# Performance work log

Measured on AMD Instinct MI355X. Metric: run time of the kernel, lower is better.

Reference implementation:

```python
import jax, jax.numpy as jnp
import numpy as np

B, T, N, C = 4, 6, 512, 8
HID, FEAT, EMB, IN_DIM = 64, 16, 32, 1
KS, KC, HORIZON = 3, 2, 3
ALPHA = 3.0

def _init(key, shape):
    fin = shape[-2] if len(shape) >= 2 else shape[-1]
    return jax.random.normal(key, shape, dtype=jnp.float32) * (1.0 / fin) ** 0.5

def setup_inputs():
    ks = jax.random.split(jax.random.key(0), 32)
    L_enc = (IN_DIM + FEAT + HID) * KS * KC
    L_dec = (HID + FEAT + HID) * KS * KC
    return {
        "X_seq": jax.random.normal(ks[0], (B, T, N, C), dtype=jnp.float32),
        "As": jax.random.uniform(ks[1], (N, N), dtype=jnp.float32) / N,
        "Ac": jax.random.uniform(ks[2], (C, C), dtype=jnp.float32) / C,
        "feature": jax.random.normal(ks[3], (N, FEAT), dtype=jnp.float32),
        "Wu_S": _init(ks[4], (C, HID)), "Wv_S": _init(ks[5], (C, HID)),
        "Wu_C": _init(ks[6], (N, HID)), "Wv_C": _init(ks[7], (N, HID)),
        "mfS_w1": _init(ks[8], (4, 2, 256)), "mfS_b1": jnp.zeros((4, 256), jnp.float32),
        "mfS_w2": _init(ks[9], (4, 256, 256)), "mfS_b2": jnp.zeros((4, 256), jnp.float32),
        "mfC_w1": _init(ks[10], (4, 2, 256)), "mfC_b1": jnp.zeros((4, 256), jnp.float32),
        "mfC_w2": _init(ks[11], (4, 256, 256)), "mfC_b2": jnp.zeros((4, 256), jnp.float32),
        "enc_gW": _init(ks[12], (L_enc, 2 * HID)), "enc_gb": jnp.zeros((2 * HID,), jnp.float32),
        "enc_cW": _init(ks[13], (L_enc, HID)), "enc_cb": jnp.zeros((HID,), jnp.float32),
        "dec_gW": _init(ks[14], (L_dec, 2 * HID)), "dec_gb": jnp.zeros((2 * HID,), jnp.float32),
        "dec_cW": _init(ks[15], (L_dec, HID)), "dec_cb": jnp.zeros((HID,), jnp.float32),
        "out_w1": _init(ks[16], (HID, EMB)), "out_b1": jnp.zeros((EMB,), jnp.float32),
        "out_w2": _init(ks[17], (EMB, IN_DIM)), "out_b2": jnp.zeros((IN_DIM,), jnp.float32),
    }

def _mlp(x, w1, b1, w2, b2):
    return jax.nn.relu(x @ w1 + b1) @ w2 + b2

def _mixed_fusion(A, P, w1, b1, w2, b2):
    # node_feat = [rowsum(A), rowsum(P)]; key/value MLPs indexed 0:key_A 1:key_P 2:val_A 3:val_P
    nf = jnp.stack([A.sum(-1), P.sum(-1)], axis=-1)            # [n, 2]
    An, Pn = A @ nf, P @ nf
    key = _mlp(An, w1[0], b1[0], w2[0], b2[0]) + _mlp(Pn, w1[1], b1[1], w2[1], b2[1])
    val = _mlp(An, w1[2], b1[2], w2[2], b2[2]) + _mlp(Pn, w1[3], b1[3], w2[3], b2[3])
    a = jax.nn.sigmoid(key @ val.T)
    return a * A + (1.0 - a) * P

def _adaptive_graph(Xf, Wu, Wv):
    U = jnp.tanh(ALPHA * Xf @ Wu)                              # [b,t,n,h]
    V = jnp.tanh(ALPHA * Xf @ Wv)
    M = jnp.einsum('btnh,btmh->nm', U, V)
    # Ps = softmax(relu(M - M^T)) matches einsum pair in torch source
    return jax.nn.softmax(jax.nn.relu(M - M.T), axis=-1)

def _cheby(G, K):
    mats = [jnp.eye(G.shape[0], dtype=G.dtype), G]
    for _ in range(2, K):
        mats.append(2.0 * G @ mats[-1] - mats[-2])
    return jnp.stack(mats[:K], axis=0)                         # [K, n, n]

def _bdg(X, Gs_set, Gc_set, W, b):
    # X: [b,n,c,l]; fused Ks x Kc Chebyshev mode products; cat order (k, j, l) matches torch cat
    t1 = jnp.einsum('bncl,knm->kbmcl', X, Gs_set)
    t2 = jnp.einsum('kbmcl,jcd->bmdkjl', t1, Gc_set)
    feat = t2.reshape(t2.shape[0], t2.shape[1], t2.shape[2], -1)
    return feat @ W + b

def _cell(Xt, Ht, featx, Gs_set, Gc_set, gW, gb, cW, cb):
    XH = jnp.concatenate([Xt, Ht, featx], axis=-1)
    uv = _bdg(XH, Gs_set, Gc_set, gW, gb)
    update = jax.nn.sigmoid(uv[..., :HID])
    reset = jax.nn.sigmoid(uv[..., HID:])
    cand_in = jnp.concatenate([Xt, reset * Ht, featx], axis=-1)
    cand = jnp.tanh(_bdg(cand_in, Gs_set, Gc_set, cW, cb))
    return (1.0 - update) * Ht + update * cand

def _forward(X_seq, As, Ac, feature, Wu_S, Wv_S, Wu_C, Wv_C,
             mfS_w1, mfS_b1, mfS_w2, mfS_b2, mfC_w1, mfC_b1, mfC_w2, mfC_b2,
             enc_gW, enc_gb, enc_cW, enc_cb, dec_gW, dec_gb, dec_cW, dec_cb,
             out_w1, out_b1, out_w2, out_b2):
    # MGP_Gen: adaptive spatial / categorical graphs fused with priors
    Ps = _adaptive_graph(X_seq, Wu_S, Wv_S)
    Gs = _mixed_fusion(As, Ps, mfS_w1, mfS_b1, mfS_w2, mfS_b2)
    Xc = jnp.swapaxes(X_seq, 2, 3)                             # [b,t,c,n]
    Pc = _adaptive_graph(Xc, Wu_C, Wv_C)
    Gc = _mixed_fusion(Ac, Pc, mfC_w1, mfC_b1, mfC_w2, mfC_b2)
    Gs_set, Gc_set = _cheby(Gs, KS), _cheby(Gc, KC)
    featx = jnp.broadcast_to(feature[None, :, None, :], (B, N, C, FEAT))
    X5 = X_seq[..., None]                                      # [b,t,n,c,1]
    Ht = jnp.zeros((B, N, C, HID), dtype=X_seq.dtype)
    for t in range(T):                                         # encoder GRU over history
        Ht = _cell(X5[:, t], Ht, featx, Gs_set, Gc_set, enc_gW, enc_gb, enc_cW, enc_cb)
    deco_in, Hd = Ht, Ht
    outs = []
    for _ in range(HORIZON):
        Hd = _cell(deco_in, Hd, featx, Gs_set, Gc_set, dec_gW, dec_gb, dec_cW, dec_cb)
        outs.append(_mlp(Hd, out_w1, out_b1, out_w2, out_b2))
        deco_in = Hd
    return jnp.stack(outs, axis=1)                             # [b, horizon, n, c, 1]

def reference(X_seq, As, Ac, feature, Wu_S, Wv_S, Wu_C, Wv_C, mfS_w1, mfS_b1, mfS_w2, mfS_b2, mfC_w1, mfC_b1, mfC_w2, mfC_b2, enc_gW, enc_gb, enc_cW, enc_cb, dec_gW, dec_gb, dec_cW, dec_cb, out_w1, out_b1, out_w2, out_b2):
    return _forward(X_seq, As, Ac, feature, Wu_S, Wv_S, Wu_C, Wv_C, mfS_w1, mfS_b1, mfS_w2, mfS_b2, mfC_w1, mfC_b1, mfC_w2, mfC_b2, enc_gW, enc_gb, enc_cW, enc_cb, dec_gW, dec_gb, dec_cW, dec_cb, out_w1, out_b1, out_w2, out_b2)
```

## Files before the change

### kernel.cpp

```cpp
#include <hip/hip_runtime.h>
#include <math.h>

constexpr int kB = 4, kT = 6, kN = 512, kC = 8;
constexpr int kH = 64, kF = 16, kE = 32;
constexpr int kKS = 3, kKC = 2, kHOR = 3;
constexpr int kBT = kB * kT;
constexpr int kRK = kBT * kH;
constexpr int L_ENC = 1 + kH + kF;
constexpr int L_DEC = kH + kH + kF;
constexpr int PL_ENC = 96;
constexpr int PL_DEC = 160;
constexpr int KP_ENC = 3 * PL_ENC;
constexpr int KP_DGF = 288;
constexpr int KP_DEC = 3 * PL_DEC;
constexpr float kALPHA = 3.0f;

typedef unsigned short ushortT;
typedef short short8 __attribute__((ext_vector_type(8)));
typedef float f32x4 __attribute__((ext_vector_type(4)));

__device__ __forceinline__ float sigm(float x) { return 1.0f / (1.0f + __expf(-x)); }

__device__ __forceinline__ ushortT f2bf(float f) {
    union { float f; unsigned int u; } v; v.f = f;
    unsigned int r = v.u + 0x7fffu + ((v.u >> 16) & 1u);
    return (ushortT)(r >> 16);
}

__device__ __forceinline__ void fma44(const float4& a, const float4& b, float acc[4][4]) {
    acc[0][0] += a.x*b.x; acc[0][1] += a.x*b.y; acc[0][2] += a.x*b.z; acc[0][3] += a.x*b.w;
    acc[1][0] += a.y*b.x; acc[1][1] += a.y*b.y; acc[1][2] += a.y*b.z; acc[1][3] += a.y*b.w;
    acc[2][0] += a.z*b.x; acc[2][1] += a.z*b.y; acc[2][2] += a.z*b.z; acc[2][3] += a.z*b.w;
    acc[3][0] += a.w*b.x; acc[3][1] += a.w*b.y; acc[3][2] += a.w*b.z; acc[3][3] += a.w*b.w;
}

__global__ __launch_bounds__(256) void k_prep_all(
    const float* __restrict__ egW, const float* __restrict__ ecW,
    const float* __restrict__ dgW, const float* __restrict__ dcW,
    const float* __restrict__ w2, const float* __restrict__ w2C,
    ushortT* __restrict__ WTg_e, ushortT* __restrict__ WTc_e,
    ushortT* __restrict__ WTg_d, ushortT* __restrict__ WTc_d,
    float* __restrict__ w2tK, float* __restrict__ w2tV, float* __restrict__ w2tC)
{
    int idx = blockIdx.x * 256 + threadIdx.x;
    if (idx < 73728) {
        int qp = idx % KP_ENC, o = idx / KP_ENC;
        int kk = qp / PL_ENC, l = qp - kk * PL_ENC;
        int lo = (l < 64) ? l + 1 : (l == 64) ? 0 : (l < 80) ? L_ENC : (l - 15);
        int j = o / 128, oo = o - j * 128;
        float v = (lo < L_ENC) ? egW[(size_t)((kk*2 + j)*L_ENC + lo) * 128 + oo] : 0.f;
        WTg_e[idx] = f2bf(v);
    } else if (idx < 110592) {
        int r = idx - 73728;
        int qp = r % KP_ENC, o = r / KP_ENC;
        int kk = qp / PL_ENC, l = qp - kk * PL_ENC;
        int lo = (l < 64) ? l + 1 : (l == 64) ? 0 : (l < 80) ? L_ENC : (l - 15);
        int j = o / 64, oo = o - j * 64;
        float v = (lo < L_ENC) ? ecW[(size_t)((kk*2 + j)*L_ENC + lo) * 64 + oo] : 0.f;
        WTc_e[r] = f2bf(v);
    } else if (idx < 184320) {
        int r = idx - 110592;
        int qp = r % KP_DGF, o = r / KP_DGF;
        int k = qp / 96, p = qp - k * 96;
        int j = o >> 7, oo = o & 127;
        int base = (k*2 + j) * L_DEC;
        float v;
        if (p < 64)      v = dgW[(size_t)(base + p)*128 + oo] + dgW[(size_t)(base + 64 + p)*128 + oo];
        else if (p < 80) v = dgW[(size_t)(base + 128 + (p - 64))*128 + oo];
        else             v = 0.f;
        WTg_d[r] = f2bf(v);
    } else if (idx < 245760) {
        int r = idx - 184320;
        int qp = r % KP_DEC, o = r / KP_DEC;
        int kk = qp / PL_DEC, l = qp - kk * PL_DEC;
        int j = o / 64, oo = o - j * 64;
        float v = (l < L_DEC) ? dcW[(size_t)((kk*2 + j)*L_DEC + l) * 64 + oo] : 0.f;
        WTc_d[r] = f2bf(v);
    } else if (idx < 376832) {
        int r = idx - 245760;
        int kk = r & 511, n = r >> 9;
        int j = kk >> 8, k = kk & 255;
        w2tK[r] = w2[(size_t)(0 + j)*65536 + k*256 + n];
        w2tV[r] = w2[(size_t)(2 + j)*65536 + k*256 + n];
    } else if (idx < 638976) {
        int r = idx - 376832;
        int q = r >> 16; int rem = r & 65535;
        int oc = rem >> 8, k = rem & 255;
        w2tC[r] = w2C[(size_t)q*65536 + k*256 + oc];
    }
}


__global__ __launch_bounds__(256) void k_uvproj_s_nfa(
    const float* __restrict__ X, const float* __restrict__ Wu, const float* __restrict__ Wv,
    const float* __restrict__ As,
    float* __restrict__ Upr, float* __restrict__ Vpr, float* __restrict__ nf)
{
    if (blockIdx.x >= 3072) {
        int i = blockIdx.x - 3072, tid = threadIdx.x;
        __shared__ float sa[256];
        float a = 0.f;
        for (int j = tid; j < kN; j += 256) a += As[(size_t)i*kN + j];
        sa[tid] = a; __syncthreads();
        for (int s = 128; s > 0; s >>= 1) { if (tid < s) sa[tid] += sa[tid+s]; __syncthreads(); }
        if (!tid) { nf[i*2] = sa[0]; nf[i*2+1] = 1.0f; }
        return;
    }
    int idx = blockIdx.x * 256 + threadIdx.x;
    int h = idx % kH; int bt = (idx / kH) % kBT; int n = idx / (kH * kBT);
    const float* xr = X + ((size_t)bt * kN + n) * kC;
    float u = 0.f, v = 0.f;
#pragma unroll
    for (int c = 0; c < kC; ++c) { float x = xr[c]; u += x * Wu[c*kH + h]; v += x * Wv[c*kH + h]; }
    Upr[(size_t)n * kRK + bt * kH + h] = tanhf(kALPHA * u);
    Vpr[(size_t)n * kRK + bt * kH + h] = tanhf(kALPHA * v);
}

__global__ __launch_bounds__(512) void k_uvproj_c2(
    const float* __restrict__ X, const float* __restrict__ WuC, const float* __restrict__ WvC,
    float* __restrict__ Uc, float* __restrict__ Vc)
{
    __shared__ float Xs[4096];
    __shared__ float Wus[4096], Wvs[4096];
    int bt = blockIdx.x, tid = threadIdx.x;
    for (int i = tid; i < 4096; i += 512) Xs[i] = X[(size_t)bt*4096 + i];
    int c = tid >> 6, h = tid & 63;
    float u = 0.f, v = 0.f;
    for (int n0 = 0; n0 < 512; n0 += 64) {
        __syncthreads();
        for (int i = tid; i < 4096; i += 512) { Wus[i] = WuC[n0*64 + i]; Wvs[i] = WvC[n0*64 + i]; }
        __syncthreads();
#pragma unroll 8
        for (int nn = 0; nn < 64; ++nn) {
            float x = Xs[(n0+nn)*8 + c];
            u += x * Wus[nn*64 + h];
            v += x * Wvs[nn*64 + h];
        }
    }
    Uc[(size_t)bt*512 + c*64 + h] = tanhf(kALPHA * u);
    Vc[(size_t)bt*512 + c*64 + h] = tanhf(kALPHA * v);
}

__global__ __launch_bounds__(256) void k_softmax_anpn(
    const float* __restrict__ part, const float* __restrict__ A, const float* __restrict__ nf,
    float* __restrict__ P, float* __restrict__ An, float* __restrict__ Pn)
{
    int i = blockIdx.x, tid = threadIdx.x;
    __shared__ float s0[256], s1[256], s2[256], s3[256], s4[256];
    auto mval = [&](int r, int c2) -> float {
        size_t id = (size_t)r*kN + c2;
        return part[id] + part[262144 + id] + part[524288 + id] + part[786432 + id];
    };
    float mx = -1e30f;
    for (int j = tid; j < kN; j += 256)
        mx = fmaxf(mx, fmaxf(mval(i, j) - mval(j, i), 0.f));
    s0[tid] = mx; __syncthreads();
    for (int s = 128; s > 0; s >>= 1) { if (tid < s) s0[tid] = fmaxf(s0[tid], s0[tid+s]); __syncthreads(); }
    mx = s0[0]; __syncthreads();
    float sum=0, pn0=0, pn1=0, an0=0, an1=0;
    for (int j = tid; j < kN; j += 256) {
        float v = fmaxf(mval(i, j) - mval(j, i), 0.f);
        float e = __expf(v - mx);
        P[(size_t)i*kN + j] = e;
        float n0 = nf[2*j], n1 = nf[2*j+1];
        float a = A[(size_t)i*kN + j];
        sum += e; pn0 += e*n0; pn1 += e*n1; an0 += a*n0; an1 += a*n1;
    }
    s0[tid]=sum; s1[tid]=pn0; s2[tid]=pn1; s3[tid]=an0; s4[tid]=an1; __syncthreads();
    for (int s = 128; s > 0; s >>= 1) {
        if (tid < s) { s0[tid]+=s0[tid+s]; s1[tid]+=s1[tid+s]; s2[tid]+=s2[tid+s]; s3[tid]+=s3[tid+s]; s4[tid]+=s4[tid+s]; }
        __syncthreads();
    }
    float inv = 1.f / s0[0];
    if (!tid) { Pn[i*2] = s1[0]*inv; Pn[i*2+1] = s2[0]*inv; An[i*2] = s3[0]; An[i*2+1] = s4[0]; }
    __syncthreads();
    for (int j = tid; j < kN; j += 256) P[(size_t)i*kN + j] *= inv;
}

__global__ __launch_bounds__(256) void k_mlp1kv(
    const float* __restrict__ An, const float* __restrict__ Pn,
    const float* __restrict__ w1, const float* __restrict__ b1, float* __restrict__ hid)
{
    int idx = blockIdx.x * 256 + threadIdx.x;
    if (idx >= 524288) return;
    int half = idx >> 18;
    int r = idx & 262143;
    int col = r & 511, i = r >> 9;
    int ia = half*2, ip = half*2 + 1;
    float v;
    if (col < 256) {
        const float* w = w1 + (size_t)ia * 512;
        v = An[i*2]*w[col] + An[i*2+1]*w[256 + col] + b1[ia*256 + col];
    } else {
        int o = col - 256;
        const float* w = w1 + (size_t)ip * 512;
        v = Pn[i*2]*w[o] + Pn[i*2+1]*w[256 + o] + b1[ip*256 + o];
    }
    hid[idx] = fmaxf(v, 0.f);
}

__global__ __launch_bounds__(256) void k_gemm_ntsk(
    const float* __restrict__ A, const float* __restrict__ B, float* __restrict__ part,
    int M, int N, int K, int skl)
{
    __shared__ __align__(16) float sA[32][68];
    __shared__ __align__(16) float sB[32][68];
    int tid = threadIdx.x, tx = tid & 15, ty = tid >> 4;
    int j0 = blockIdx.x * 64, i0 = blockIdx.y * 64;
    int kb = blockIdx.z * skl;
    float acc[4][4] = {};
    for (int k0 = kb; k0 < kb + skl; k0 += 32) {
#pragma unroll
        for (int it = 0; it < 2; ++it) {
            int q = tid + it * 256;
            int row = q >> 3, ks = (q & 7) * 4;
            float4 va = *(const float4*)&A[(size_t)(i0 + row)*K + k0 + ks];
            float4 vb = *(const float4*)&B[(size_t)(j0 + row)*K + k0 + ks];
            sA[ks+0][row] = va.x; sA[ks+1][row] = va.y; sA[ks+2][row] = va.z; sA[ks+3][row] = va.w;
            sB[ks+0][row] = vb.x; sB[ks+1][row] = vb.y; sB[ks+2][row] = vb.z; sB[ks+3][row] = vb.w;
        }
        __syncthreads();
#pragma unroll
        for (int kk = 0; kk < 32; ++kk) {
            float4 a = *(const float4*)&sA[kk][ty*4];
            float4 b = *(const float4*)&sB[kk][tx*4];
            fma44(a, b, acc);
        }
        __syncthreads();
    }
    float* dst = part + (size_t)blockIdx.z * M * N;
#pragma unroll
    for (int i = 0; i < 4; ++i)
#pragma unroll
        for (int j = 0; j < 4; ++j)
            dst[(size_t)(i0 + ty*4 + i)*N + j0 + tx*4 + j] = acc[i][j];
}

__global__ __launch_bounds__(256) void k_ntsk_kv2(
    const float* __restrict__ hid, const float* __restrict__ w2t,
    const float* __restrict__ b2, float* __restrict__ keyval)
{
    __shared__ __align__(16) float sA[32][68];
    __shared__ __align__(16) float sB[32][68];
    int tid = threadIdx.x, tx = tid & 15, ty = tid >> 4;
    int z = blockIdx.z;
    const float* A = hid + (size_t)z * 262144;
    const float* B = w2t + (size_t)z * 131072;
    int j0 = blockIdx.x * 64, i0 = blockIdx.y * 64;
    float acc[4][4] = {};
    for (int k0 = 0; k0 < 512; k0 += 32) {
#pragma unroll
        for (int it = 0; it < 2; ++it) {
            int q = tid + it * 256;
            int row = q >> 3, ks = (q & 7) * 4;
            float4 va = *(const float4*)&A[(size_t)(i0 + row)*512 + k0 + ks];
            float4 vb = *(const float4*)&B[(size_t)(j0 + row)*512 + k0 + ks];
            sA[ks+0][row] = va.x; sA[ks+1][row] = va.y; sA[ks+2][row] = va.z; sA[ks+3][row] = va.w;
            sB[ks+0][row] = vb.x; sB[ks+1][row] = vb.y; sB[ks+2][row] = vb.z; sB[ks+3][row] = vb.w;
        }
        __syncthreads();
#pragma unroll
        for (int kk = 0; kk < 32; ++kk) {
            float4 a = *(const float4*)&sA[kk][ty*4];
            float4 b = *(const float4*)&sB[kk][tx*4];
            fma44(a, b, acc);
        }
        __syncthreads();
    }
    float* dst = keyval + (size_t)z * 131072;
#pragma unroll
    for (int i = 0; i < 4; ++i)
#pragma unroll
        for (int j = 0; j < 4; ++j) {
            int col = j0 + tx*4 + j;
            dst[(size_t)(i0 + ty*4 + i)*256 + col] = acc[i][j] + b2[z*512 + col] + b2[z*512 + 256 + col];
        }
}

__global__ void k_fuse_transp(
    const float* __restrict__ part, const float* __restrict__ As,
    const float* __restrict__ Ps, ushortT* __restrict__ Gt)
{
    __shared__ float tile[32][33];
    int bx = blockIdx.x * 32, by = blockIdx.y * 32;
    int x = threadIdx.x, y0 = threadIdx.y;
    for (int yy = y0; yy < 32; yy += 8) {
        size_t id = (size_t)(by + yy)*kN + bx + x;
        float s = part[id] + part[262144 + id];
        float a = sigm(s);
        tile[yy][x] = a*As[id] + (1.f - a)*Ps[id];
    }
    __syncthreads();
    for (int yy = y0; yy < 32; yy += 8) Gt[(size_t)(bx+yy)*kN + by + x] = f2bf(tile[x][yy]);
}

__global__ __launch_bounds__(256) void k_cheby64(
    const ushortT* __restrict__ Gst, ushortT* __restrict__ Gst2)
{
    __shared__ short sA[64][40];
    __shared__ short sB[64][40];
    int tid = threadIdx.x;
    int m0 = blockIdx.y * 64, j0 = blockIdx.x * 64;
    int w = tid >> 6, lane = tid & 63;
    f32x4 acc[4];
#pragma unroll
    for (int i = 0; i < 4; ++i) acc[i] = (f32x4){0.f, 0.f, 0.f, 0.f};
    for (int k0 = 0; k0 < kN; k0 += 32) {
        {
            int row = tid >> 2, lc = (tid & 3) * 8;
            *(short8*)&sA[row][lc] = *(const short8*)(Gst + (size_t)(m0 + row)*kN + k0 + lc);
        }
        {
            int kr = tid & 31, jc = (tid >> 5) * 8;
            short8 v = *(const short8*)(Gst + (size_t)(k0 + kr)*kN + j0 + jc);
#pragma unroll
            for (int i = 0; i < 8; ++i) sB[jc + i][kr] = v[i];
        }
        __syncthreads();
        short8 bf = *(const short8*)&sB[w*16 + (lane & 15)][(lane >> 4) * 8];
#pragma unroll
        for (int mi = 0; mi < 4; ++mi) {
            short8 af = *(const short8*)&sA[mi*16 + (lane & 15)][(lane >> 4) * 8];
            acc[mi] = __builtin_amdgcn_mfma_f32_16x16x32_bf16(af, bf, acc[mi], 0, 0, 0);
        }
        __syncthreads();
    }
#pragma unroll
    for (int mi = 0; mi < 4; ++mi) {
        int row0 = m0 + mi*16 + (lane >> 4)*4;
        int col = j0 + w*16 + (lane & 15);
#pragma unroll
        for (int q = 0; q < 4; ++q) {
            int row = row0 + q;
            Gst2[(size_t)row*kN + col] = f2bf(2.f*acc[mi][q] - (row == col ? 1.f : 0.f));
        }
    }
}

__device__ __forceinline__ void cat_front2(
    const float* __restrict__ Uc, const float* __restrict__ Vc, const float* __restrict__ Ac,
    float* UVs , float* red ,
    float* McS, float* Pcs, float* rsA, float* Ans, float* Pns)
{
    int tid = threadIdx.x;
    int cd = tid >> 2, kc = tid & 3;
    int c = cd >> 3, d = cd & 7;
    float s = 0.f;
    for (int bt0 = 0; bt0 < kBT; bt0 += 4) {
        __syncthreads();
        for (int i = tid; i < 2048; i += 256) {
            UVs[i]        = Uc[(size_t)bt0*512 + i];
            UVs[2048 + i] = Vc[(size_t)bt0*512 + i];
        }
        __syncthreads();
#pragma unroll
        for (int bt = 0; bt < 4; ++bt)
#pragma unroll
            for (int hh = 0; hh < 16; ++hh) {
                int h = kc*16 + hh;
                s += UVs[bt*512 + c*64 + h] * UVs[2048 + bt*512 + d*64 + h];
            }
    }
    red[tid] = s; __syncthreads();
    if (tid < 64) McS[tid] = red[tid*4] + red[tid*4+1] + red[tid*4+2] + red[tid*4+3];
    __syncthreads();
    if (tid < 8) {
        int i = tid;
        float row[8]; float mx = -1e30f;
#pragma unroll
        for (int j = 0; j < 8; ++j) { float v = fmaxf(McS[i*8+j] - McS[j*8+i], 0.f); row[j] = v; mx = fmaxf(mx, v); }
        float s2 = 0.f;
#pragma unroll
        for (int j = 0; j < 8; ++j) { row[j] = __expf(row[j] - mx); s2 += row[j]; }
        float inv = 1.f / s2;
#pragma unroll
        for (int j = 0; j < 8; ++j) Pcs[i*8+j] = row[j] * inv;
        float a = 0.f;
#pragma unroll
        for (int j = 0; j < 8; ++j) a += Ac[i*8+j];
        rsA[i] = a;
    }
    __syncthreads();
    if (tid < 16) {
        int i = tid >> 1, comp = tid & 1;
        float an = 0.f, pn = 0.f;
#pragma unroll
        for (int j = 0; j < 8; ++j) {
            float nfj = comp ? 1.f : rsA[j];
            an += Ac[i*8+j] * nfj; pn += Pcs[i*8+j] * nfj;
        }
        Ans[i*2+comp] = an; Pns[i*2+comp] = pn;
    }
    __syncthreads();
}

__global__ __launch_bounds__(256) void k_catmlp4(
    const float* __restrict__ Uc, const float* __restrict__ Vc, const float* __restrict__ Ac,
    const float* __restrict__ w1, const float* __restrict__ b1,
    const float* __restrict__ w2tC, const float* __restrict__ b2,
    float* __restrict__ keyval)
{
    __shared__ float UVs[4096];
    __shared__ float red[256];
    __shared__ float McS[64], Pcs[64], rsA[8], Ans[16], Pns[16];
    __shared__ float hA[8][260], hP[8][260];
    int tid = threadIdx.x;
    int kv = blockIdx.x, c0 = blockIdx.y * 32;
    int qa = kv*2, qp = kv*2 + 1;
    cat_front2(Uc, Vc, Ac, UVs, red, McS, Pcs, rsA, Ans, Pns);
    for (int e = tid; e < 2048; e += 256) {
        int i = e >> 8, o = e & 255;
        hA[i][o] = fmaxf(Ans[i*2]*w1[qa*512 + o] + Ans[i*2+1]*w1[qa*512 + 256 + o] + b1[qa*256 + o], 0.f);
        hP[i][o] = fmaxf(Pns[i*2]*w1[qp*512 + o] + Pns[i*2+1]*w1[qp*512 + 256 + o] + b1[qp*256 + o], 0.f);
    }
    __syncthreads();
    int i = tid >> 5, ocl = tid & 31, oc = c0 + ocl;
    float s = b2[qa*256 + oc] + b2[qp*256 + oc];
    const float* wa = w2tC + (size_t)qa*65536 + (size_t)oc*256;
    const float* wp = w2tC + (size_t)qp*65536 + (size_t)oc*256;
#pragma unroll 4
    for (int k = 0; k < 256; k += 4) {
        float4 va = *(const float4*)&wa[k];
        float4 vp = *(const float4*)&wp[k];
        float4 ha = *(const float4*)&hA[i][k];
        float4 hp = *(const float4*)&hP[i][k];
        s += va.x*ha.x + va.y*ha.y + va.z*ha.z + va.w*ha.w
           + vp.x*hp.x + vp.y*hp.y + vp.z*hp.z + vp.w*hp.w;
    }
    keyval[(size_t)kv*2048 + i*256 + oc] = s;
}

__global__ __launch_bounds__(256) void k_gcfuse4(
    const float* __restrict__ keyval,
    const float* __restrict__ Uc, const float* __restrict__ Vc, const float* __restrict__ Ac,
    float* __restrict__ GcF)
{
    __shared__ float UVs[4096];
    __shared__ float red[256];
    __shared__ float McS[64], Pcs[64], rsA[8], Ans[16], Pns[16];
    __shared__ float dotp[256];
    int tid = threadIdx.x;
    cat_front2(Uc, Vc, Ac, UVs, red, McS, Pcs, rsA, Ans, Pns);
    int cd = tid >> 2, kc = tid & 3;
    int c = cd >> 3, d = cd & 7;
    const float* key = keyval;
    const float* val = keyval + 2048;
    float s = 0.f;
#pragma unroll 4
    for (int k = kc*64; k < kc*64 + 64; k += 4) {
        float4 k4 = *(const float4*)&key[c*256 + k];
        float4 v4 = *(const float4*)&val[d*256 + k];
        s += k4.x*v4.x + k4.y*v4.y + k4.z*v4.z + k4.w*v4.w;
    }
    dotp[tid] = s; __syncthreads();
    if (tid < 64) {
        float t = dotp[tid*4] + dotp[tid*4+1] + dotp[tid*4+2] + dotp[tid*4+3];
        float a = sigm(t);
        GcF[tid] = a*Ac[tid] + (1.f - a)*Pcs[tid];
    }
}

template<int CLP, int PL, int ACTW, int OFF>
__global__ __launch_bounds__(256) void k_t1m(
    const ushortT* __restrict__ Gst, const ushortT* __restrict__ Xin, ushortT* __restrict__ Yout)
{
    __shared__ short sA[128][40];
    __shared__ short sB[128][40];
    int tid = threadIdx.x;
    int ki = blockIdx.z >> 2, b = blockIdx.z & 3;
    const ushortT* A = Gst + (size_t)ki * kN * kN;
    const ushortT* B = Xin + (size_t)b * kN * CLP;
    ushortT* C = Yout + (size_t)(ki*4 + b) * kN * CLP;
    int m0 = blockIdx.y * 128, j0 = blockIdx.x * 128;
    int w = tid >> 6, lane = tid & 63, wr = w >> 1, wc = w & 1;
    int kr = tid & 31, jc = (tid >> 5) * 8;
    int colr0, colr1;
    { int j = j0 + jc;      int cg = j / ACTW; colr0 = cg*PL + OFF + (j - cg*ACTW); }
    { int j = j0 + jc + 64; int cg = j / ACTW; colr1 = cg*PL + OFF + (j - cg*ACTW); }
    f32x4 acc[4][4];
#pragma unroll
    for (int i = 0; i < 4; ++i)
#pragma unroll
        for (int j = 0; j < 4; ++j) acc[i][j] = (f32x4){0.f, 0.f, 0.f, 0.f};

    for (int k0 = 0; k0 < kN; k0 += 32) {
        {
            int row = tid >> 1, lc = (tid & 1) * 16;
            const ushortT* p = A + (size_t)(m0 + row)*kN + k0 + lc;
            *(short8*)&sA[row][lc]     = *(const short8*)p;
            *(short8*)&sA[row][lc + 8] = *(const short8*)(p + 8);
        }
        {
            short8 v0 = *(const short8*)(B + (size_t)(k0 + kr)*CLP + colr0);
            short8 v1 = *(const short8*)(B + (size_t)(k0 + kr)*CLP + colr1);
#pragma unroll
            for (int i = 0; i < 8; ++i) sB[jc + i][kr] = v0[i];
#pragma unroll
            for (int i = 0; i < 8; ++i) sB[jc + 64 + i][kr] = v1[i];
        }
        __syncthreads();
        short8 af[4], bfr[4];
#pragma unroll
        for (int mi = 0; mi < 4; ++mi)
            af[mi] = *(const short8*)&sA[wr*64 + mi*16 + (lane & 15)][(lane >> 4) * 8];
#pragma unroll
        for (int ni = 0; ni < 4; ++ni)
            bfr[ni] = *(const short8*)&sB[wc*64 + ni*16 + (lane & 15)][(lane >> 4) * 8];
#pragma unroll
        for (int mi = 0; mi < 4; ++mi)
#pragma unroll
            for (int ni = 0; ni < 4; ++ni)
                acc[mi][ni] = __builtin_amdgcn_mfma_f32_16x16x32_bf16(af[mi], bfr[ni], acc[mi][ni], 0, 0, 0);
        __syncthreads();
    }
#pragma unroll
    for (int mi = 0; mi < 4; ++mi) {
#pragma unroll
        for (int ni = 0; ni < 4; ++ni) {
            int row = m0 + wr*64 + mi*16 + (lane >> 4) * 4;
            int fj = j0 + wc*64 + ni*16;
            int cg = fj / ACTW;
            int col = cg*PL + OFF + (fj - cg*ACTW) + (lane & 15);
#pragma unroll
            for (int q = 0; q < 4; ++q)
                C[(size_t)(row + q)*CLP + col] = f2bf(acc[mi][ni][q]);
        }
    }
}

template<int PL, int NQ, int MODE, int FN>
__global__ __launch_bounds__(256) void k_gg(
    const ushortT* __restrict__ XH, const ushortT* __restrict__ Yb,
    const ushortT* __restrict__ WT, float* __restrict__ Cout)
{
    constexpr int BN = 32 * FN;
    constexpr int KP = NQ * 32;
    constexpr int Ntot = 64 * FN;
    __shared__ short sA[128][40];
    __shared__ short sB[BN][40];
    int tid = threadIdx.x;
    int r0 = blockIdx.y * 128, j0 = blockIdx.x * BN;
    int b = r0 >> 12, rr = r0 & 4095;
    const ushortT* src0 = XH + (size_t)r0 * PL;
    const ushortT* src1 = Yb + ((size_t)b       * 4096 + rr) * PL;
    const ushortT* src2 = Yb + ((size_t)(4 + b) * 4096 + rr) * PL;
    int w = tid >> 6, lane = tid & 63, wr = w >> 1, wc = w & 1;
    f32x4 acc[4][FN];
#pragma unroll
    for (int i = 0; i < 4; ++i)
#pragma unroll
        for (int j = 0; j < FN; ++j) acc[i][j] = (f32x4){0.f, 0.f, 0.f, 0.f};

    for (int q = 0; q < NQ; ++q) {
        int k, off;
        if (MODE == 0)      { k = q/3; off = (q - k*3)*32; }
        else if (MODE == 1) { k = q/3; int part = q - k*3; off = (part < 2) ? part*32 : 128; }
        else                { k = q/5; off = (q - k*5)*32; }
        const ushortT* Ap = (k == 0) ? src0 : (k == 1) ? src1 : src2;
        {
            int row = tid >> 1, lc = (tid & 1) * 16;
            const ushortT* p = Ap + (size_t)row * PL + off + lc;
            *(short8*)&sA[row][lc]     = *(const short8*)p;
            *(short8*)&sA[row][lc + 8] = *(const short8*)(p + 8);
        }
        if (FN == 4) {
            int col = tid >> 1, seg = (tid & 1) * 16;
            const ushortT* p = WT + (size_t)(j0 + col)*KP + q*32 + seg;
            *(short8*)&sB[col][seg]     = *(const short8*)p;
            *(short8*)&sB[col][seg + 8] = *(const short8*)(p + 8);
        } else {
            int col = tid >> 2, seg = (tid & 3) * 8;
            *(short8*)&sB[col][seg] = *(const short8*)(WT + (size_t)(j0 + col)*KP + q*32 + seg);
        }
        __syncthreads();
        short8 af[4], bfr[FN];
#pragma unroll
        for (int mi = 0; mi < 4; ++mi)
            af[mi] = *(const short8*)&sA[wr*64 + mi*16 + (lane & 15)][(lane >> 4) * 8];
#pragma unroll
        for (int ni = 0; ni < FN; ++ni)
            bfr[ni] = *(const short8*)&sB[wc*16*FN + ni*16 + (lane & 15)][(lane >> 4) * 8];
#pragma unroll
        for (int mi = 0; mi < 4; ++mi)
#pragma unroll
            for (int ni = 0; ni < FN; ++ni)
                acc[mi][ni] = __builtin_amdgcn_mfma_f32_16x16x32_bf16(af[mi], bfr[ni], acc[mi][ni], 0, 0, 0);
        __syncthreads();
    }
#pragma unroll
    for (int mi = 0; mi < 4; ++mi) {
#pragma unroll
        for (int ni = 0; ni < FN; ++ni) {
            int row = r0 + wr*64 + mi*16 + (lane >> 4) * 4;
            int col = j0 + wc*16*FN + ni*16 + (lane & 15);
#pragma unroll
            for (int q = 0; q < 4; ++q)
                Cout[(size_t)(row + q)*Ntot + col] = acc[mi][ni][q];
        }
    }
}


template<int PL, int XOFF>
__global__ __launch_bounds__(256) void k_gates_ep(
    const float* __restrict__ Gg, const float* __restrict__ GcM,
    const float* __restrict__ gb, const float* __restrict__ Ht,
    float* __restrict__ upd, ushortT* __restrict__ XH)
{
    __shared__ float sG[8][256];
    __shared__ float GcS[64];
    int tid = threadIdx.x, bm = blockIdx.x;
    const float* src = Gg + (size_t)bm * 2048;
    for (int i = tid; i < 2048; i += 256) sG[i >> 8][i & 255] = src[i];
    if (tid < 64) GcS[tid] = GcM[tid];
    __syncthreads();
    int d = tid >> 5, o0 = (tid & 31) * 4;
    size_t rb = (size_t)bm * 8 + d;
#pragma unroll
    for (int q = 0; q < 4; ++q) {
        int o = o0 + q;
        float pre = sG[d][o] + gb[o];
#pragma unroll
        for (int c = 0; c < 8; ++c) pre += GcS[c*8 + d] * sG[c][128 + o];
        float g = sigm(pre);
        if (o < kH) upd[rb*kH + o] = g;
        else {
            int h = o - kH;
            XH[rb*PL + XOFF + h] = f2bf(g * Ht[rb*kH + h]);
        }
    }
}

template<int MODE>
__global__ __launch_bounds__(256) void k_cand_ep(
    const float* __restrict__ Gc2, const float* __restrict__ GcM,
    const float* __restrict__ cb, const float* __restrict__ upd,
    float* __restrict__ Ht, ushortT* __restrict__ XHo,
    const float* __restrict__ X, int tnext,
    const float* __restrict__ ow1, const float* __restrict__ ob1,
    const float* __restrict__ ow2, const float* __restrict__ ob2,
    float* __restrict__ out, int hz)
{
    __shared__ float sG[8][128];
    __shared__ float GcS[64];
    __shared__ float Hn[8][65];
    __shared__ float Pp[8][32];
    int tid = threadIdx.x, bm = blockIdx.x;
    const float* src = Gc2 + (size_t)bm * 1024;
    for (int i = tid; i < 1024; i += 256) sG[i >> 7][i & 127] = src[i];
    if (tid < 64) GcS[tid] = GcM[tid];
    __syncthreads();
    int d = tid >> 5, o0 = (tid & 31) * 2;
    size_t rb = (size_t)bm * 8 + d;
#pragma unroll
    for (int jj = 0; jj < 2; ++jj) {
        int o = o0 + jj;
        float pre = sG[d][o] + cb[o];
#pragma unroll
        for (int c = 0; c < 8; ++c) pre += GcS[c*8 + d] * sG[c][64 + o];
        float cv = tanhf(pre);
        float u = upd[rb*kH + o];
        float h0 = Ht[rb*kH + o];
        float hn = (1.f - u)*h0 + u*cv;
        Ht[rb*kH + o] = hn;
        if (MODE >= 2) Hn[d][o] = hn;
        if (MODE == 0)      XHo[rb*PL_ENC + o] = f2bf(hn);
        else if (MODE <= 2) XHo[rb*PL_DEC + o] = f2bf(hn);
    }
    if (MODE == 0) {
        if (tid < 8) {
            int r = bm*8 + tid;
            int c2 = r & 7, m = (r >> 3) & 511, b2 = r >> 12;
            XHo[(size_t)r*PL_ENC + 64] = f2bf(X[(((size_t)b2*kT + tnext)*kN + m)*kC + c2]);
        }
    }
    if (MODE >= 2) {
        __syncthreads();
        int row = tid >> 5, e = tid & 31;
        float s = ob1[e];
#pragma unroll
        for (int k = 0; k < kH; ++k) s += Hn[row][k] * ow1[k*kE + e];
        Pp[row][e] = fmaxf(s, 0.f) * ow2[e];
        __syncthreads();
        if (tid < 8) {
            float v = ob2[0];
#pragma unroll
            for (int e2 = 0; e2 < 32; ++e2) v += Pp[tid][e2];
            int r = bm*8 + tid;
            int c2 = r & 7, m = (r >> 3) & 511, b2 = r >> 12;
            out[((size_t)(b2*kHOR + hz)*kN + m)*kC + c2] = v;
        }
    }
}

__global__ __launch_bounds__(256) void k_build_init(
    const float* __restrict__ X, const float* __restrict__ featr,
    ushortT* __restrict__ XHe, ushortT* __restrict__ XHd, float* __restrict__ Ht)
{
    int idx = blockIdx.x * 256 + threadIdx.x;
    if (idx < 1572864) {
        int l = idx % PL_ENC; int r = idx / PL_ENC;
        float v;
        if (l < 64)       v = 0.f;
        else if (l == 64) { int c = r & 7, m = (r >> 3) & 511, b = r >> 12; v = X[(((size_t)b*kT)*kN + m)*kC + c]; }
        else if (l < 80)  v = 0.f;
        else              { int m = (r >> 3) & 511; v = featr[m*kF + (l - 80)]; }
        XHe[idx] = f2bf(v);
    } else if (idx < 2097152) {
        int r2 = idx - 1572864;
        int l2 = r2 & 31; int r = r2 >> 5;
        float v = (l2 < 16) ? featr[((r >> 3) & 511)*kF + l2] : 0.f;
        XHd[(size_t)r*PL_DEC + 128 + l2] = f2bf(v);
    } else if (idx < 3145728) {
        Ht[idx - 2097152] = 0.f;
    }
}

extern "C" void kernel_launch(void* const* d_in, const int* in_sizes, int n_in,
                              void* d_out, int out_size, void* d_ws, size_t ws_size,
                              hipStream_t stream)
{
    (void)in_sizes; (void)n_in; (void)out_size; (void)ws_size;
    const float* X      = (const float*)d_in[0];
    const float* As     = (const float*)d_in[1];
    const float* Ac     = (const float*)d_in[2];
    const float* featr  = (const float*)d_in[3];
    const float* WuS    = (const float*)d_in[4];
    const float* WvS    = (const float*)d_in[5];
    const float* WuC    = (const float*)d_in[6];
    const float* WvC    = (const float*)d_in[7];
    const float* mfS_w1 = (const float*)d_in[8];
    const float* mfS_b1 = (const float*)d_in[9];
    const float* mfS_w2 = (const float*)d_in[10];
    const float* mfS_b2 = (const float*)d_in[11];
    const float* mfC_w1 = (const float*)d_in[12];
    const float* mfC_b1 = (const float*)d_in[13];
    const float* mfC_w2 = (const float*)d_in[14];
    const float* mfC_b2 = (const float*)d_in[15];
    const float* enc_gW = (const float*)d_in[16];
    const float* enc_gb = (const float*)d_in[17];
    const float* enc_cW = (const float*)d_in[18];
    const float* enc_cb = (const float*)d_in[19];
    const float* dec_gW = (const float*)d_in[20];
    const float* dec_gb = (const float*)d_in[21];
    const float* dec_cW = (const float*)d_in[22];
    const float* dec_cb = (const float*)d_in[23];
    const float* out_w1 = (const float*)d_in[24];
    const float* out_b1 = (const float*)d_in[25];
    const float* out_w2 = (const float*)d_in[26];
    const float* out_b2 = (const float*)d_in[27];
    float* out = (float*)d_out;
    float* ws = (float*)d_ws;

    float* Ht     = ws;
    float* updb   = Ht + 1048576;
    float* Gg     = updb + 1048576;
    float* Gs_pad = Gg + 4194304;
    float* smallf = Gs_pad + 262144;
    float* nfS = smallf;
    float* AnS = nfS + 1024;
    float* PnS = AnS + 1024;
    float* GcF = PnS + 1024;
    float* kvC = GcF + 64;
    ushortT* XHb  = (ushortT*)(smallf + 8192);
    ushortT* Yb   = XHb + 2621440;
    ushortT* GstB = Yb + 5242880;
    ushortT* WTg_e = GstB + 524288;
    ushortT* WTc_e = WTg_e + 73728;
    ushortT* WTg_d = WTc_e + 36864;
    ushortT* WTc_d = WTg_d + 122880;
    ushortT* XHd   = WTc_d + 61440;
    float* Upr   = Gg;
    float* Vpr   = Upr + 786432;
    float* part  = Vpr + 786432;
    float* Ps    = part + 1048576;
    float* hidKV = Ps + 262144;
    float* keyval= hidKV + 524288;
    float* w2tKV = keyval + 262144;
    float* w2tC  = w2tKV + 262144;
    float* Uc    = updb;
    float* Vc    = Uc + 12288;

    constexpr int CLP_ENC = kC * PL_ENC;
    constexpr int CLP_DEC = kC * PL_DEC;

    k_prep_all<<<2496, 256, 0, stream>>>(enc_gW, enc_cW, dec_gW, dec_cW, mfS_w2, mfC_w2,
                                         WTg_e, WTc_e, WTg_d, WTc_d,
                                         w2tKV, w2tKV + 131072, w2tC);

    k_uvproj_s_nfa<<<3584, 256, 0, stream>>>(X, WuS, WvS, As, Upr, Vpr, nfS);
    k_gemm_ntsk<<<dim3(8, 8, 4), 256, 0, stream>>>(Upr, Vpr, part, 512, 512, 1536, 384);
    k_softmax_anpn<<<kN, 256, 0, stream>>>(part, As, nfS, Ps, AnS, PnS);
    k_mlp1kv<<<2048, 256, 0, stream>>>(AnS, PnS, mfS_w1, mfS_b1, hidKV);
    k_ntsk_kv2<<<dim3(4, 8, 2), 256, 0, stream>>>(hidKV, w2tKV, mfS_b2, keyval);
    k_gemm_ntsk<<<dim3(8, 8, 2), 256, 0, stream>>>(keyval, keyval + 131072, part, 512, 512, 256, 128);
    k_fuse_transp<<<dim3(16, 16), dim3(32, 8), 0, stream>>>(part, As, Ps, GstB);
    k_cheby64<<<dim3(8, 8), 256, 0, stream>>>(GstB, GstB + 262144);

    k_uvproj_c2<<<kBT, 512, 0, stream>>>(X, WuC, WvC, Uc, Vc);
    k_catmlp4<<<dim3(2, 8), 256, 0, stream>>>(Uc, Vc, Ac, mfC_w1, mfC_b1, w2tC, mfC_b2, kvC);
    k_gcfuse4<<<1, 256, 0, stream>>>(kvC, Uc, Vc, Ac, GcF);

    k_build_init<<<12288, 256, 0, stream>>>(X, featr, XHb, XHd, Ht);

    for (int t = 0; t < kT; ++t) {
        if (t == 0)
            k_t1m<CLP_ENC, PL_ENC, 96, 0><<<dim3(6, 4, 8), 256, 0, stream>>>(GstB, XHb, Yb);
        else
            k_t1m<CLP_ENC, PL_ENC, 80, 0><<<dim3(5, 4, 8), 256, 0, stream>>>(GstB, XHb, Yb);
        k_gg<PL_ENC, 9, 0, 4><<<dim3(2, 128), 256, 0, stream>>>(XHb, Yb, WTg_e, Gg);
        k_gates_ep<PL_ENC, 0><<<2048, 256, 0, stream>>>(Gg, GcF, enc_gb, Ht, updb, XHb);
        k_t1m<CLP_ENC, PL_ENC, 64, 0><<<dim3(4, 4, 8), 256, 0, stream>>>(GstB, XHb, Yb);
        k_gg<PL_ENC, 9, 0, 2><<<dim3(2, 128), 256, 0, stream>>>(XHb, Yb, WTc_e, Gg);
        if (t < kT - 1)
            k_cand_ep<0><<<2048, 256, 0, stream>>>(Gg, GcF, enc_cb, updb, Ht, XHb, X, t + 1,
                                                   nullptr, nullptr, nullptr, nullptr, nullptr, 0);
        else
            k_cand_ep<1><<<2048, 256, 0, stream>>>(Gg, GcF, enc_cb, updb, Ht, XHd, nullptr, 0,
                                                   nullptr, nullptr, nullptr, nullptr, nullptr, 0);
    }

    k_t1m<CLP_DEC, PL_DEC, 16, 128><<<dim3(1, 4, 8), 256, 0, stream>>>(GstB, XHd, Yb);
    for (int hz = 0; hz < kHOR; ++hz) {
        k_t1m<CLP_DEC, PL_DEC, 64, 0><<<dim3(4, 4, 8), 256, 0, stream>>>(GstB, XHd, Yb);
        k_gg<PL_DEC, 9, 1, 4><<<dim3(2, 128), 256, 0, stream>>>(XHd, Yb, WTg_d, Gg);
        k_gates_ep<PL_DEC, 64><<<2048, 256, 0, stream>>>(Gg, GcF, dec_gb, Ht, updb, XHd);
        k_t1m<CLP_DEC, PL_DEC, 64, 64><<<dim3(4, 4, 8), 256, 0, stream>>>(GstB, XHd, Yb);
        k_gg<PL_DEC, 15, 2, 2><<<dim3(2, 128), 256, 0, stream>>>(XHd, Yb, WTc_d, Gg);
        if (hz < kHOR - 1)
            k_cand_ep<2><<<2048, 256, 0, stream>>>(Gg, GcF, dec_cb, updb, Ht, XHd, nullptr, 0,
                                                   out_w1, out_b1, out_w2, out_b2, out, hz);
        else
            k_cand_ep<3><<<2048, 256, 0, stream>>>(Gg, GcF, dec_cb, updb, Ht, XHd, nullptr, 0,
                                                   out_w1, out_b1, out_w2, out_b2, out, hz);
    }
}
```

Measured before the change: 926.0 us.

## Merge front-end prep kernels and fuse spatial/channel graph stages into fewer launches

Folds weight prep, spatial and channel UV projections, row sums and state init into a single k_front launch. The Upr·Vpr partial GEMM is merged with the channel cat-MLP in k_p2, and the softmax is merged with the channel gate fusion in k_p3. In the decoder, the static feature-column product is folded into the first gate-side graph multiply through extra blocks. The aim is fewer kernel launches and serial dependency points, with independent work running concurrently inside one grid. The cost is heterogeneous blocks in each launch and shared-memory unions that may limit occupancy.

New measurement: 916.2 us. No clear change (-1.0%).

```diff
diff --git a/kernel.cpp b/kernel.cpp
--- a/kernel.cpp
+++ b/kernel.cpp
@@ -34,148 +34,323 @@
     acc[3][0] += a.w*b.x; acc[3][1] += a.w*b.y; acc[3][2] += a.w*b.z; acc[3][3] += a.w*b.w;
 }
 
-__global__ __launch_bounds__(256) void k_prep_all(
+__global__ __launch_bounds__(256) void k_front(
     const float* __restrict__ egW, const float* __restrict__ ecW,
     const float* __restrict__ dgW, const float* __restrict__ dcW,
     const float* __restrict__ w2, const float* __restrict__ w2C,
+    const float* __restrict__ X, const float* __restrict__ Wu, const float* __restrict__ Wv,
+    const float* __restrict__ As, const float* __restrict__ WuC, const float* __restrict__ WvC,
+    const float* __restrict__ featr,
     ushortT* __restrict__ WTg_e, ushortT* __restrict__ WTc_e,
     ushortT* __restrict__ WTg_d, ushortT* __restrict__ WTc_d,
-    float* __restrict__ w2tK, float* __restrict__ w2tV, float* __restrict__ w2tC)
-{
-    int idx = blockIdx.x * 256 + threadIdx.x;
-    if (idx < 73728) {
-        int qp = idx % KP_ENC, o = idx / KP_ENC;
-        int kk = qp / PL_ENC, l = qp - kk * PL_ENC;
-        int lo = (l < 64) ? l + 1 : (l == 64) ? 0 : (l < 80) ? L_ENC : (l - 15);
-        int j = o / 128, oo = o - j * 128;
-        float v = (lo < L_ENC) ? egW[(size_t)((kk*2 + j)*L_ENC + lo) * 128 + oo] : 0.f;
-        WTg_e[idx] = f2bf(v);
-    } else if (idx < 110592) {
-        int r = idx - 73728;
-        int qp = r % KP_ENC, o = r / KP_ENC;
-        int kk = qp / PL_ENC, l = qp - kk * PL_ENC;
-        int lo = (l < 64) ? l + 1 : (l == 64) ? 0 : (l < 80) ? L_ENC : (l - 15);
-        int j = o / 64, oo = o - j * 64;
-        float v = (lo < L_ENC) ? ecW[(size_t)((kk*2 + j)*L_ENC + lo) * 64 + oo] : 0.f;
-        WTc_e[r] = f2bf(v);
-    } else if (idx < 184320) {
-        int r = idx - 110592;
-        int qp = r % KP_DGF, o = r / KP_DGF;
-        int k = qp / 96, p = qp - k * 96;
-        int j = o >> 7, oo = o & 127;
-        int base = (k*2 + j) * L_DEC;
-        float v;
-        if (p < 64)      v = dgW[(size_t)(base + p)*128 + oo] + dgW[(size_t)(base + 64 + p)*128 + oo];
-        else if (p < 80) v = dgW[(size_t)(base + 128 + (p - 64))*128 + oo];
-        else             v = 0.f;
-        WTg_d[r] = f2bf(v);
-    } else if (idx < 245760) {
-        int r = idx - 184320;
-        int qp = r % KP_DEC, o = r / KP_DEC;
-        int kk = qp / PL_DEC, l = qp - kk * PL_DEC;
-        int j = o / 64, oo = o - j * 64;
-        float v = (l < L_DEC) ? dcW[(size_t)((kk*2 + j)*L_DEC + l) * 64 + oo] : 0.f;
-        WTc_d[r] = f2bf(v);
-    } else if (idx < 376832) {
-        int r = idx - 245760;
-        int kk = r & 511, n = r >> 9;
-        int j = kk >> 8, k = kk & 255;
-        w2tK[r] = w2[(size_t)(0 + j)*65536 + k*256 + n];
-        w2tV[r] = w2[(size_t)(2 + j)*65536 + k*256 + n];
-    } else if (idx < 638976) {
-        int r = idx - 376832;
-        int q = r >> 16; int rem = r & 65535;
-        int oc = rem >> 8, k = rem & 255;
-        w2tC[r] = w2C[(size_t)q*65536 + k*256 + oc];
-    }
-}
-
-
-__global__ __launch_bounds__(256) void k_uvproj_s_nfa(
-    const float* __restrict__ X, const float* __restrict__ Wu, const float* __restrict__ Wv,
-    const float* __restrict__ As,
-    float* __restrict__ Upr, float* __restrict__ Vpr, float* __restrict__ nf)
-{
-    if (blockIdx.x >= 3072) {
-        int i = blockIdx.x - 3072, tid = threadIdx.x;
-        __shared__ float sa[256];
+    float* __restrict__ w2tK, float* __restrict__ w2tV, float* __restrict__ w2tC,
+    float* __restrict__ Upr, float* __restrict__ Vpr, float* __restrict__ nf,
+    float* __restrict__ Uc, float* __restrict__ Vc,
+    ushortT* __restrict__ XHe, ushortT* __restrict__ XHd, float* __restrict__ Ht)
+{
+    __shared__ float shmem[4096];
+    int blk = blockIdx.x, tid = threadIdx.x;
+    if (blk < 2496) {
+        int idx = blk * 256 + tid;
+        if (idx < 73728) {
+            int qp = idx % KP_ENC, o = idx / KP_ENC;
+            int kk = qp / PL_ENC, l = qp - kk * PL_ENC;
+            int lo = (l < 64) ? l + 1 : (l == 64) ? 0 : (l < 80) ? L_ENC : (l - 15);
+            int j = o / 128, oo = o - j * 128;
+            float v = (lo < L_ENC) ? egW[(size_t)((kk*2 + j)*L_ENC + lo) * 128 + oo] : 0.f;
+            WTg_e[idx] = f2bf(v);
+        } else if (idx < 110592) {
+            int r = idx - 73728;
+            int qp = r % KP_ENC, o = r / KP_ENC;
+            int kk = qp / PL_ENC, l = qp - kk * PL_ENC;
+            int lo = (l < 64) ? l + 1 : (l == 64) ? 0 : (l < 80) ? L_ENC : (l - 15);
+            int j = o / 64, oo = o - j * 64;
+            float v = (lo < L_ENC) ? ecW[(size_t)((kk*2 + j)*L_ENC + lo) * 64 + oo] : 0.f;
+            WTc_e[r] = f2bf(v);
+        } else if (idx < 184320) {
+            int r = idx - 110592;
+            int qp = r % KP_DGF, o = r / KP_DGF;
+            int k = qp / 96, p = qp - k * 96;
+            int j = o >> 7, oo = o & 127;
+            int base = (k*2 + j) * L_DEC;
+            float v;
+            if (p < 64)      v = dgW[(size_t)(base + p)*128 + oo] + dgW[(size_t)(base + 64 + p)*128 + oo];
+            else if (p < 80) v = dgW[(size_t)(base + 128 + (p - 64))*128 + oo];
+            else             v = 0.f;
+            WTg_d[r] = f2bf(v);
+        } else if (idx < 245760) {
+            int r = idx - 184320;
+            int qp = r % KP_DEC, o = r / KP_DEC;
+            int kk = qp / PL_DEC, l = qp - kk * PL_DEC;
+            int j = o / 64, oo = o - j * 64;
+            float v = (l < L_DEC) ? dcW[(size_t)((kk*2 + j)*L_DEC + l) * 64 + oo] : 0.f;
+            WTc_d[r] = f2bf(v);
+        } else if (idx < 376832) {
+            int r = idx - 245760;
+            int kk = r & 511, n = r >> 9;
+            int j = kk >> 8, k = kk & 255;
+            w2tK[r] = w2[(size_t)(0 + j)*65536 + k*256 + n];
+            w2tV[r] = w2[(size_t)(2 + j)*65536 + k*256 + n];
+        } else if (idx < 638976) {
+            int r = idx - 376832;
+            int q = r >> 16; int rem = r & 65535;
+            int oc = rem >> 8, k = rem & 255;
+            w2tC[r] = w2C[(size_t)q*65536 + k*256 + oc];
+        }
+    } else if (blk < 6080) {
+        int b2 = blk - 2496;
+        if (b2 >= 3072) {
+            int i = b2 - 3072;
+            float* sa = shmem;
+            float a = 0.f;
+            for (int j = tid; j < kN; j += 256) a += As[(size_t)i*kN + j];
+            sa[tid] = a; __syncthreads();
+            for (int s = 128; s > 0; s >>= 1) { if (tid < s) sa[tid] += sa[tid+s]; __syncthreads(); }
+            if (!tid) { nf[i*2] = sa[0]; nf[i*2+1] = 1.0f; }
+            return;
+        }
+        int idx = b2 * 256 + tid;
+        int h = idx % kH; int bt = (idx / kH) % kBT; int n = idx / (kH * kBT);
+        const float* xr = X + ((size_t)bt * kN + n) * kC;
+        float u = 0.f, v = 0.f;
+#pragma unroll
+        for (int c = 0; c < kC; ++c) { float x = xr[c]; u += x * Wu[c*kH + h]; v += x * Wv[c*kH + h]; }
+        Upr[(size_t)n * kRK + bt * kH + h] = tanhf(kALPHA * u);
+        Vpr[(size_t)n * kRK + bt * kH + h] = tanhf(kALPHA * v);
+    } else if (blk < 6104) {
+        int bt = blk - 6080;
+        float* Xs = shmem;
+        for (int i = tid; i < 4096; i += 256) Xs[i] = X[(size_t)bt*4096 + i];
+        __syncthreads();
+        int c = tid >> 6, h = tid & 63;
+        float u0 = 0.f, v0 = 0.f, u1 = 0.f, v1 = 0.f;
+        for (int n = 0; n < 512; ++n) {
+            float wu = WuC[n*64 + h], wv = WvC[n*64 + h];
+            float x0 = Xs[n*8 + c], x1 = Xs[n*8 + c + 4];
+            u0 += x0*wu; v0 += x0*wv; u1 += x1*wu; v1 += x1*wv;
+        }
+        Uc[(size_t)bt*512 + c*64 + h]       = tanhf(kALPHA * u0);
+        Vc[(size_t)bt*512 + c*64 + h]       = tanhf(kALPHA * v0);
+        Uc[(size_t)bt*512 + (c+4)*64 + h]   = tanhf(kALPHA * u1);
+        Vc[(size_t)bt*512 + (c+4)*64 + h]   = tanhf(kALPHA * v1);
+    } else {
+        int idx = (blk - 6104) * 256 + tid;
+        if (idx < 1572864) {
+            int l = idx % PL_ENC; int r = idx / PL_ENC;
+            float v;
+            if (l < 64)       v = 0.f;
+            else if (l == 64) { int c = r & 7, m = (r >> 3) & 511, b = r >> 12; v = X[(((size_t)b*kT)*kN + m)*kC + c]; }
+            else if (l < 80)  v = 0.f;
+            else              { int m = (r >> 3) & 511; v = featr[m*kF + (l - 80)]; }
+            XHe[idx] = f2bf(v);
+        } else if (idx < 2097152) {
+            int r2 = idx - 1572864;
+            int l2 = r2 & 31; int r = r2 >> 5;
+            float v = (l2 < 16) ? featr[((r >> 3) & 511)*kF + l2] : 0.f;
+            XHd[(size_t)r*PL_DEC + 128 + l2] = f2bf(v);
+        } else if (idx < 3145728) {
+            Ht[idx - 2097152] = 0.f;
+        }
+    }
+}
+
+__device__ __forceinline__ void cat_front2(
+    const float* __restrict__ Uc, const float* __restrict__ Vc, const float* __restrict__ Ac,
+    float* UVs, float* red, float* McS, float* Pcs, float* rsA, float* Ans, float* Pns)
+{
+    int tid = threadIdx.x;
+    int cd = tid >> 2, kc = tid & 3;
+    int c = cd >> 3, d = cd & 7;
+    float s = 0.f;
+    for (int bt0 = 0; bt0 < kBT; bt0 += 4) {
+        __syncthreads();
+        for (int i = tid; i < 2048; i += 256) {
+            UVs[i]        = Uc[(size_t)bt0*512 + i];
+            UVs[2048 + i] = Vc[(size_t)bt0*512 + i];
+        }
+        __syncthreads();
+#pragma unroll
+        for (int bt = 0; bt < 4; ++bt)
+#pragma unroll
+            for (int hh = 0; hh < 16; ++hh) {
+                int h = kc*16 + hh;
+                s += UVs[bt*512 + c*64 + h] * UVs[2048 + bt*512 + d*64 + h];
+            }
+    }
+    red[tid] = s; __syncthreads();
+    if (tid < 64) McS[tid] = red[tid*4] + red[tid*4+1] + red[tid*4+2] + red[tid*4+3];
+    __syncthreads();
+    if (tid < 8) {
+        int i = tid;
+        float row[8]; float mx = -1e30f;
+#pragma unroll
+        for (int j = 0; j < 8; ++j) { float v = fmaxf(McS[i*8+j] - McS[j*8+i], 0.f); row[j] = v; mx = fmaxf(mx, v); }
+        float s2 = 0.f;
+#pragma unroll
+        for (int j = 0; j < 8; ++j) { row[j] = __expf(row[j] - mx); s2 += row[j]; }
+        float inv = 1.f / s2;
+#pragma unroll
+        for (int j = 0; j < 8; ++j) Pcs[i*8+j] = row[j] * inv;
         float a = 0.f;
-        for (int j = tid; j < kN; j += 256) a += As[(size_t)i*kN + j];
-        sa[tid] = a; __syncthreads();
-        for (int s = 128; s > 0; s >>= 1) { if (tid < s) sa[tid] += sa[tid+s]; __syncthreads(); }
-        if (!tid) { nf[i*2] = sa[0]; nf[i*2+1] = 1.0f; }
-        return;
-    }
-    int idx = blockIdx.x * 256 + threadIdx.x;
-    int h = idx % kH; int bt = (idx / kH) % kBT; int n = idx / (kH * kBT);
-    const float* xr = X + ((size_t)bt * kN + n) * kC;
-    float u = 0.f, v = 0.f;
-#pragma unroll
-    for (int c = 0; c < kC; ++c) { float x = xr[c]; u += x * Wu[c*kH + h]; v += x * Wv[c*kH + h]; }
-    Upr[(size_t)n * kRK + bt * kH + h] = tanhf(kALPHA * u);
-    Vpr[(size_t)n * kRK + bt * kH + h] = tanhf(kALPHA * v);
-}
-
-__global__ __launch_bounds__(512) void k_uvproj_c2(
-    const float* __restrict__ X, const float* __restrict__ WuC, const float* __restrict__ WvC,
-    float* __restrict__ Uc, float* __restrict__ Vc)
-{
-    __shared__ float Xs[4096];
-    __shared__ float Wus[4096], Wvs[4096];
-    int bt = blockIdx.x, tid = threadIdx.x;
-    for (int i = tid; i < 4096; i += 512) Xs[i] = X[(size_t)bt*4096 + i];
-    int c = tid >> 6, h = tid & 63;
-    float u = 0.f, v = 0.f;
-    for (int n0 = 0; n0 < 512; n0 += 64) {
-        __syncthreads();
-        for (int i = tid; i < 4096; i += 512) { Wus[i] = WuC[n0*64 + i]; Wvs[i] = WvC[n0*64 + i]; }
-        __syncthreads();
-#pragma unroll 8
-        for (int nn = 0; nn < 64; ++nn) {
-            float x = Xs[(n0+nn)*8 + c];
-            u += x * Wus[nn*64 + h];
-            v += x * Wvs[nn*64 + h];
-        }
-    }
-    Uc[(size_t)bt*512 + c*64 + h] = tanhf(kALPHA * u);
-    Vc[(size_t)bt*512 + c*64 + h] = tanhf(kALPHA * v);
-}
-
-__global__ __launch_bounds__(256) void k_softmax_anpn(
+#pragma unroll
+        for (int j = 0; j < 8; ++j) a += Ac[i*8+j];
+        rsA[i] = a;
+    }
+    __syncthreads();
+    if (tid < 16) {
+        int i = tid >> 1, comp = tid & 1;
+        float an = 0.f, pn = 0.f;
+#pragma unroll
+        for (int j = 0; j < 8; ++j) {
+            float nfj = comp ? 1.f : rsA[j];
+            an += Ac[i*8+j] * nfj; pn += Pcs[i*8+j] * nfj;
+        }
+        Ans[i*2+comp] = an; Pns[i*2+comp] = pn;
+    }
+    __syncthreads();
+}
+
+union P2Smem {
+    struct { float sA[32][68]; float sB[32][68]; } g;
+    struct { float UVs[4096]; float red[256]; float McS[64]; float Pcs[64]; float rsA[8];
+             float Ans[16]; float Pns[16]; float hA[8][260]; float hP[8][260]; } c;
+};
+
+__global__ __launch_bounds__(256) void k_p2(
+    const float* __restrict__ Upr, const float* __restrict__ Vpr, float* __restrict__ part,
+    const float* __restrict__ Uc, const float* __restrict__ Vc, const float* __restrict__ Ac,
+    const float* __restrict__ w1, const float* __restrict__ b1,
+    const float* __restrict__ w2tC, const float* __restrict__ b2c,
+    float* __restrict__ keyval)
+{
+    __shared__ P2Smem sm;
+    int tid = threadIdx.x;
+    if (blockIdx.x < 256) {
+        int x = blockIdx.x & 7, y = (blockIdx.x >> 3) & 7, z = blockIdx.x >> 6;
+        int tx = tid & 15, ty = tid >> 4;
+        int j0 = x * 64, i0 = y * 64;
+        int kb = z * 384;
+        float acc[4][4] = {};
+        for (int k0 = kb; k0 < kb + 384; k0 += 32) {
+#pragma unroll
+            for (int it = 0; it < 2; ++it) {
+                int q = tid + it * 256;
+                int row = q >> 3, ks = (q & 7) * 4;
+                float4 va = *(const float4*)&Upr[(size_t)(i0 + row)*1536 + k0 + ks];
+                float4 vb = *(const float4*)&Vpr[(size_t)(j0 + row)*1536 + k0 + ks];
+                sm.g.sA[ks+0][row] = va.x; sm.g.sA[ks+1][row] = va.y; sm.g.sA[ks+2][row] = va.z; sm.g.sA[ks+3][row] = va.w;
+                sm.g.sB[ks+0][row] = vb.x; sm.g.sB[ks+1][row] = vb.y; sm.g.sB[ks+2][row] = vb.z; sm.g.sB[ks+3][row] = vb.w;
+            }
+            __syncthreads();
+#pragma unroll
+            for (int kk = 0; kk < 32; ++kk) {
+                float4 a = *(const float4*)&sm.g.sA[kk][ty*4];
+                float4 b = *(const float4*)&sm.g.sB[kk][tx*4];
+                fma44(a, b, acc);
+            }
+            __syncthreads();
+        }
+        float* dst = part + (size_t)z * 262144;
+#pragma unroll
+        for (int i = 0; i < 4; ++i)
+#pragma unroll
+            for (int j = 0; j < 4; ++j)
+                dst[(size_t)(i0 + ty*4 + i)*512 + j0 + tx*4 + j] = acc[i][j];
+    } else {
+        int r = blockIdx.x - 256;
+        int kv = r & 1, c0 = (r >> 1) * 32;
+        int qa = kv*2, qp = kv*2 + 1;
+        cat_front2(Uc, Vc, Ac, sm.c.UVs, sm.c.red, sm.c.McS, sm.c.Pcs, sm.c.rsA, sm.c.Ans, sm.c.Pns);
+        for (int e = tid; e < 2048; e += 256) {
+            int i = e >> 8, o = e & 255;
+            sm.c.hA[i][o] = fmaxf(sm.c.Ans[i*2]*w1[qa*512 + o] + sm.c.Ans[i*2+1]*w1[qa*512 + 256 + o] + b1[qa*256 + o], 0.f);
+            sm.c.hP[i][o] = fmaxf(sm.c.Pns[i*2]*w1[qp*512 + o] + sm.c.Pns[i*2+1]*w1[qp*512 + 256 + o] + b1[qp*256 + o], 0.f);
+        }
+        __syncthreads();
+        int i = tid >> 5, ocl = tid & 31, oc = c0 + ocl;
+        float s = b2c[qa*256 + oc] + b2c[qp*256 + oc];
+        const float* wa = w2tC + (size_t)qa*65536 + (size_t)oc*256;
+        const float* wp = w2tC + (size_t)qp*65536 + (size_t)oc*256;
+#pragma unroll 4
+        for (int k = 0; k < 256; k += 4) {
+            float4 va = *(const float4*)&wa[k];
+            float4 vp = *(const float4*)&wp[k];
+            float4 ha = *(const float4*)&sm.c.hA[i][k];
+            float4 hp = *(const float4*)&sm.c.hP[i][k];
+            s += va.x*ha.x + va.y*ha.y + va.z*ha.z + va.w*ha.w
+               + vp.x*hp.x + vp.y*hp.y + vp.z*hp.z + vp.w*hp.w;
+        }
+        keyval[(size_t)kv*2048 + i*256 + oc] = s;
+    }
+}
+
+union P3Smem {
+    struct { float s0[256]; float s1[256]; float s2[256]; float s3[256]; float s4[256]; } s;
+    struct { float UVs[4096]; float red[256]; float McS[64]; float Pcs[64]; float rsA[8];
+             float Ans[16]; float Pns[16]; float dotp[256]; } c;
+};
+
+__global__ __launch_bounds__(256) void k_p3(
     const float* __restrict__ part, const float* __restrict__ A, const float* __restrict__ nf,
-    float* __restrict__ P, float* __restrict__ An, float* __restrict__ Pn)
-{
-    int i = blockIdx.x, tid = threadIdx.x;
-    __shared__ float s0[256], s1[256], s2[256], s3[256], s4[256];
-    auto mval = [&](int r, int c2) -> float {
-        size_t id = (size_t)r*kN + c2;
-        return part[id] + part[262144 + id] + part[524288 + id] + part[786432 + id];
-    };
-    float mx = -1e30f;
-    for (int j = tid; j < kN; j += 256)
-        mx = fmaxf(mx, fmaxf(mval(i, j) - mval(j, i), 0.f));
-    s0[tid] = mx; __syncthreads();
-    for (int s = 128; s > 0; s >>= 1) { if (tid < s) s0[tid] = fmaxf(s0[tid], s0[tid+s]); __syncthreads(); }
-    mx = s0[0]; __syncthreads();
-    float sum=0, pn0=0, pn1=0, an0=0, an1=0;
-    for (int j = tid; j < kN; j += 256) {
-        float v = fmaxf(mval(i, j) - mval(j, i), 0.f);
-        float e = __expf(v - mx);
-        P[(size_t)i*kN + j] = e;
-        float n0 = nf[2*j], n1 = nf[2*j+1];
-        float a = A[(size_t)i*kN + j];
-        sum += e; pn0 += e*n0; pn1 += e*n1; an0 += a*n0; an1 += a*n1;
-    }
-    s0[tid]=sum; s1[tid]=pn0; s2[tid]=pn1; s3[tid]=an0; s4[tid]=an1; __syncthreads();
-    for (int s = 128; s > 0; s >>= 1) {
-        if (tid < s) { s0[tid]+=s0[tid+s]; s1[tid]+=s1[tid+s]; s2[tid]+=s2[tid+s]; s3[tid]+=s3[tid+s]; s4[tid]+=s4[tid+s]; }
-        __syncthreads();
-    }
-    float inv = 1.f / s0[0];
-    if (!tid) { Pn[i*2] = s1[0]*inv; Pn[i*2+1] = s2[0]*inv; An[i*2] = s3[0]; An[i*2+1] = s4[0]; }
-    __syncthreads();
-    for (int j = tid; j < kN; j += 256) P[(size_t)i*kN + j] *= inv;
-}
+    float* __restrict__ P, float* __restrict__ An, float* __restrict__ Pn,
+    const float* __restrict__ keyval,
+    const float* __restrict__ Uc, const float* __restrict__ Vc, const float* __restrict__ Ac,
+    float* __restrict__ GcF)
+{
+    __shared__ P3Smem sm;
+    int tid = threadIdx.x;
+    if (blockIdx.x < 512) {
+        int i = blockIdx.x;
+        auto mval = [&](int r, int c2) -> float {
+            size_t id = (size_t)r*kN + c2;
+            return part[id] + part[262144 + id] + part[524288 + id] + part[786432 + id];
+        };
+        float mx = -1e30f;
+        for (int j = tid; j < kN; j += 256)
+            mx = fmaxf(mx, fmaxf(mval(i, j) - mval(j, i), 0.f));
+        sm.s.s0[tid] = mx; __syncthreads();
+        for (int s = 128; s > 0; s >>= 1) { if (tid < s) sm.s.s0[tid] = fmaxf(sm.s.s0[tid], sm.s.s0[tid+s]); __syncthreads(); }
+        mx = sm.s.s0[0]; __syncthreads();
+        float sum=0, pn0=0, pn1=0, an0=0, an1=0;
+        for (int j = tid; j < kN; j += 256) {
+            float v = fmaxf(mval(i, j) - mval(j, i), 0.f);
+            float e = __expf(v - mx);
+            P[(size_t)i*kN + j] = e;
+            float n0 = nf[2*j], n1 = nf[2*j+1];
+            float a = A[(size_t)i*kN + j];
+            sum += e; pn0 += e*n0; pn1 += e*n1; an0 += a*n0; an1 += a*n1;
+        }
+        sm.s.s0[tid]=sum; sm.s.s1[tid]=pn0; sm.s.s2[tid]=pn1; sm.s.s3[tid]=an0; sm.s.s4[tid]=an1; __syncthreads();
+        for (int s = 128; s > 0; s >>= 1) {
+            if (tid < s) { sm.s.s0[tid]+=sm.s.s0[tid+s]; sm.s.s1[tid]+=sm.s.s1[tid+s]; sm.s.s2[tid]+=sm.s.s2[tid+s]; sm.s.s3[tid]+=sm.s.s3[tid+s]; sm.s.s4[tid]+=sm.s.s4[tid+s]; }
+            __syncthreads();
+        }
+        float inv = 1.f / sm.s.s0[0];
+        if (!tid) { Pn[i*2] = sm.s.s1[0]*inv; Pn[i*2+1] = sm.s.s2[0]*inv; An[i*2] = sm.s.s3[0]; An[i*2+1] = sm.s.s4[0]; }
+        __syncthreads();
+        for (int j = tid; j < kN; j += 256) P[(size_t)i*kN + j] *= inv;
+    } else {
+        cat_front2(Uc, Vc, Ac, sm.c.UVs, sm.c.red, sm.c.McS, sm.c.Pcs, sm.c.rsA, sm.c.Ans, sm.c.Pns);
+        int cd = tid >> 2, kc = tid & 3;
+        int c = cd >> 3, d = cd & 7;
+        const float* key = keyval;
+        const float* val = keyval + 2048;
+        float s = 0.f;
+#pragma unroll 4
+        for (int k = kc*64; k < kc*64 + 64; k += 4) {
+            float4 k4 = *(const float4*)&key[c*256 + k];
+            float4 v4 = *(const float4*)&val[d*256 + k];
+            s += k4.x*v4.x + k4.y*v4.y + k4.z*v4.z + k4.w*v4.w;
+        }
+        sm.c.dotp[tid] = s; __syncthreads();
+        if (tid < 64) {
+            float t = sm.c.dotp[tid*4] + sm.c.dotp[tid*4+1] + sm.c.dotp[tid*4+2] + sm.c.dotp[tid*4+3];
+            float a = sigm(t);
+            GcF[tid] = a*Ac[tid] + (1.f - a)*sm.c.Pcs[tid];
+        }
+    }
+}
+
 
 __global__ __launch_bounds__(256) void k_mlp1kv(
     const float* __restrict__ An, const float* __restrict__ Pn,
@@ -337,129 +512,6 @@
     }
 }
 
-__device__ __forceinline__ void cat_front2(
-    const float* __restrict__ Uc, const float* __restrict__ Vc, const float* __restrict__ Ac,
-    float* UVs , float* red ,
-    float* McS, float* Pcs, float* rsA, float* Ans, float* Pns)
-{
-    int tid = threadIdx.x;
-    int cd = tid >> 2, kc = tid & 3;
-    int c = cd >> 3, d = cd & 7;
-    float s = 0.f;
-    for (int bt0 = 0; bt0 < kBT; bt0 += 4) {
-        __syncthreads();
-        for (int i = tid; i < 2048; i += 256) {
-            UVs[i]        = Uc[(size_t)bt0*512 + i];
-            UVs[2048 + i] = Vc[(size_t)bt0*512 + i];
-        }
-        __syncthreads();
-#pragma unroll
-        for (int bt = 0; bt < 4; ++bt)
-#pragma unroll
-            for (int hh = 0; hh < 16; ++hh) {
-                int h = kc*16 + hh;
-                s += UVs[bt*512 + c*64 + h] * UVs[2048 + bt*512 + d*64 + h];
-            }
-    }
-    red[tid] = s; __syncthreads();
-    if (tid < 64) McS[tid] = red[tid*4] + red[tid*4+1] + red[tid*4+2] + red[tid*4+3];
-    __syncthreads();
-    if (tid < 8) {
-        int i = tid;
-        float row[8]; float mx = -1e30f;
-#pragma unroll
-        for (int j = 0; j < 8; ++j) { float v = fmaxf(McS[i*8+j] - McS[j*8+i], 0.f); row[j] = v; mx = fmaxf(mx, v); }
-        float s2 = 0.f;
-#pragma unroll
-        for (int j = 0; j < 8; ++j) { row[j] = __expf(row[j] - mx); s2 += row[j]; }
-        float inv = 1.f / s2;
-#pragma unroll
-        for (int j = 0; j < 8; ++j) Pcs[i*8+j] = row[j] * inv;
-        float a = 0.f;
-#pragma unroll
-        for (int j = 0; j < 8; ++j) a += Ac[i*8+j];
-        rsA[i] = a;
-    }
-    __syncthreads();
-    if (tid < 16) {
-        int i = tid >> 1, comp = tid & 1;
-        float an = 0.f, pn = 0.f;
-#pragma unroll
-        for (int j = 0; j < 8; ++j) {
-            float nfj = comp ? 1.f : rsA[j];
-            an += Ac[i*8+j] * nfj; pn += Pcs[i*8+j] * nfj;
-        }
-        Ans[i*2+comp] = an; Pns[i*2+comp] = pn;
-    }
-    __syncthreads();
-}
-
-__global__ __launch_bounds__(256) void k_catmlp4(
-    const float* __restrict__ Uc, const float* __restrict__ Vc, const float* __restrict__ Ac,
-    const float* __restrict__ w1, const float* __restrict__ b1,
-    const float* __restrict__ w2tC, const float* __restrict__ b2,
-    float* __restrict__ keyval)
-{
-    __shared__ float UVs[4096];
-    __shared__ float red[256];
-    __shared__ float McS[64], Pcs[64], rsA[8], Ans[16], Pns[16];
-    __shared__ float hA[8][260], hP[8][260];
-    int tid = threadIdx.x;
-    int kv = blockIdx.x, c0 = blockIdx.y * 32;
-    int qa = kv*2, qp = kv*2 + 1;
-    cat_front2(Uc, Vc, Ac, UVs, red, McS, Pcs, rsA, Ans, Pns);
-    for (int e = tid; e < 2048; e += 256) {
-        int i = e >> 8, o = e & 255;
-        hA[i][o] = fmaxf(Ans[i*2]*w1[qa*512 + o] + Ans[i*2+1]*w1[qa*512 + 256 + o] + b1[qa*256 + o], 0.f);
-        hP[i][o] = fmaxf(Pns[i*2]*w1[qp*512 + o] + Pns[i*2+1]*w1[qp*512 + 256 + o] + b1[qp*256 + o], 0.f);
-    }
-    __syncthreads();
-    int i = tid >> 5, ocl = tid & 31, oc = c0 + ocl;
-    float s = b2[qa*256 + oc] + b2[qp*256 + oc];
-    const float* wa = w2tC + (size_t)qa*65536 + (size_t)oc*256;
-    const float* wp = w2tC + (size_t)qp*65536 + (size_t)oc*256;
-#pragma unroll 4
-    for (int k = 0; k < 256; k += 4) {
-        float4 va = *(const float4*)&wa[k];
-        float4 vp = *(const float4*)&wp[k];
-        float4 ha = *(const float4*)&hA[i][k];
-        float4 hp = *(const float4*)&hP[i][k];
-        s += va.x*ha.x + va.y*ha.y + va.z*ha.z + va.w*ha.w
-           + vp.x*hp.x + vp.y*hp.y + vp.z*hp.z + vp.w*hp.w;
-    }
-    keyval[(size_t)kv*2048 + i*256 + oc] = s;
-}
-
-__global__ __launch_bounds__(256) void k_gcfuse4(
-    const float* __restrict__ keyval,
-    const float* __restrict__ Uc, const float* __restrict__ Vc, const float* __restrict__ Ac,
-    float* __restrict__ GcF)
-{
-    __shared__ float UVs[4096];
-    __shared__ float red[256];
-    __shared__ float McS[64], Pcs[64], rsA[8], Ans[16], Pns[16];
-    __shared__ float dotp[256];
-    int tid = threadIdx.x;
-    cat_front2(Uc, Vc, Ac, UVs, red, McS, Pcs, rsA, Ans, Pns);
-    int cd = tid >> 2, kc = tid & 3;
-    int c = cd >> 3, d = cd & 7;
-    const float* key = keyval;
-    const float* val = keyval + 2048;
-    float s = 0.f;
-#pragma unroll 4
-    for (int k = kc*64; k < kc*64 + 64; k += 4) {
-        float4 k4 = *(const float4*)&key[c*256 + k];
-        float4 v4 = *(const float4*)&val[d*256 + k];
-        s += k4.x*v4.x + k4.y*v4.y + k4.z*v4.z + k4.w*v4.w;
-    }
-    dotp[tid] = s; __syncthreads();
-    if (tid < 64) {
-        float t = dotp[tid*4] + dotp[tid*4+1] + dotp[tid*4+2] + dotp[tid*4+3];
-        float a = sigm(t);
-        GcF[tid] = a*Ac[tid] + (1.f - a)*Pcs[tid];
-    }
-}
-
 template<int CLP, int PL, int ACTW, int OFF>
 __global__ __launch_bounds__(256) void k_t1m(
     const ushortT* __restrict__ Gst, const ushortT* __restrict__ Xin, ushortT* __restrict__ Yout)
@@ -528,6 +580,77 @@
     }
 }
 
+__global__ __launch_bounds__(256) void k_t1m_decg(
+    const ushortT* __restrict__ Gst, const ushortT* __restrict__ Xin, ushortT* __restrict__ Yout)
+{
+    constexpr int CLP = 1280, PL = 160;
+    __shared__ short sA[128][40];
+    __shared__ short sB[128][40];
+    int tid = threadIdx.x;
+    int ki = blockIdx.z >> 2, b = blockIdx.z & 3;
+    const ushortT* A = Gst + (size_t)ki * kN * kN;
+    const ushortT* B = Xin + (size_t)b * kN * CLP;
+    ushortT* C = Yout + (size_t)(ki*4 + b) * kN * CLP;
+    int ACTW, OFF, j0;
+    if (blockIdx.x < 4) { ACTW = 64; OFF = 0; j0 = blockIdx.x * 128; }
+    else                { ACTW = 16; OFF = 128; j0 = 0; }
+    int m0 = blockIdx.y * 128;
+    int w = tid >> 6, lane = tid & 63, wr = w >> 1, wc = w & 1;
+    int kr = tid & 31, jc = (tid >> 5) * 8;
+    int colr0, colr1;
+    { int j = j0 + jc;      int cg = j / ACTW; colr0 = cg*PL + OFF + (j - cg*ACTW); }
+    { int j = j0 + jc + 64; int cg = j / ACTW; colr1 = cg*PL + OFF + (j - cg*ACTW); }
+    f32x4 acc[4][4];
+#pragma unroll
+    for (int i = 0; i < 4; ++i)
+#pragma unroll
+        for (int j = 0; j < 4; ++j) acc[i][j] = (f32x4){0.f, 0.f, 0.f, 0.f};
+
+    for (int k0 = 0; k0 < kN; k0 += 32) {
+        {
+            int row = tid >> 1, lc = (tid & 1) * 16;
+            const ushortT* p = A + (size_t)(m0 + row)*kN + k0 + lc;
+            *(short8*)&sA[row][lc]     = *(const short8*)p;
+            *(short8*)&sA[row][lc + 8] = *(const short8*)(p + 8);
+        }
+        {
+            short8 v0 = *(const short8*)(B + (size_t)(k0 + kr)*CLP + colr0);
+            short8 v1 = *(const short8*)(B + (size_t)(k0 + kr)*CLP + colr1);
+#pragma unroll
+            for (int i = 0; i < 8; ++i) sB[jc + i][kr] = v0[i];
+#pragma unroll
+            for (int i = 0; i < 8; ++i) sB[jc + 64 + i][kr] = v1[i];
+        }
+        __syncthreads();
+        short8 af[4], bfr[4];
+#pragma unroll
+        for (int mi = 0; mi < 4; ++mi)
+            af[mi] = *(const short8*)&sA[wr*64 + mi*16 + (lane & 15)][(lane >> 4) * 8];
+#pragma unroll
+        for (int ni = 0; ni < 4; ++ni)
+            bfr[ni] = *(const short8*)&sB[wc*64 + ni*16 + (lane & 15)][(lane >> 4) * 8];
+#pragma unroll
+        for (int mi = 0; mi < 4; ++mi)
+#pragma unroll
+            for (int ni = 0; ni < 4; ++ni)
+                acc[mi][ni] = __builtin_amdgcn_mfma_f32_16x16x32_bf16(af[mi], bfr[ni], acc[mi][ni], 0, 0, 0);
+        __syncthreads();
+    }
+#pragma unroll
+    for (int mi = 0; mi < 4; ++mi) {
+#pragma unroll
+        for (int ni = 0; ni < 4; ++ni) {
+            int row = m0 + wr*64 + mi*16 + (lane >> 4) * 4;
+            int fj = j0 + wc*64 + ni*16;
+            int cg = fj / ACTW;
+            int col = cg*PL + OFF + (fj - cg*ACTW) + (lane & 15);
+#pragma unroll
+            for (int q = 0; q < 4; ++q)
+                C[(size_t)(row + q)*CLP + col] = f2bf(acc[mi][ni][q]);
+        }
+    }
+}
+
 template<int PL, int NQ, int MODE, int FN>
 __global__ __launch_bounds__(256) void k_gg(
     const ushortT* __restrict__ XH, const ushortT* __restrict__ Yb,
@@ -690,29 +813,6 @@
             int c2 = r & 7, m = (r >> 3) & 511, b2 = r >> 12;
             out[((size_t)(b2*kHOR + hz)*kN + m)*kC + c2] = v;
         }
-    }
-}
-
-__global__ __launch_bounds__(256) void k_build_init(
-    const float* __restrict__ X, const float* __restrict__ featr,
-    ushortT* __restrict__ XHe, ushortT* __restrict__ XHd, float* __restrict__ Ht)
-{
-    int idx = blockIdx.x * 256 + threadIdx.x;
-    if (idx < 1572864) {
-        int l = idx % PL_ENC; int r = idx / PL_ENC;
-        float v;
-        if (l < 64)       v = 0.f;
-        else if (l == 64) { int c = r & 7, m = (r >> 3) & 511, b = r >> 12; v = X[(((size_t)b*kT)*kN + m)*kC + c]; }
-        else if (l < 80)  v = 0.f;
-        else              { int m = (r >> 3) & 511; v = featr[m*kF + (l - 80)]; }
-        XHe[idx] = f2bf(v);
-    } else if (idx < 2097152) {
-        int r2 = idx - 1572864;
-        int l2 = r2 & 31; int r = r2 >> 5;
-        float v = (l2 < 16) ? featr[((r >> 3) & 511)*kF + l2] : 0.f;
-        XHd[(size_t)r*PL_DEC + 128 + l2] = f2bf(v);
-    } else if (idx < 3145728) {
-        Ht[idx - 2097152] = 0.f;
     }
 }
 
@@ -784,24 +884,20 @@
     constexpr int CLP_ENC = kC * PL_ENC;
     constexpr int CLP_DEC = kC * PL_DEC;
 
-    k_prep_all<<<2496, 256, 0, stream>>>(enc_gW, enc_cW, dec_gW, dec_cW, mfS_w2, mfC_w2,
-                                         WTg_e, WTc_e, WTg_d, WTc_d,
-                                         w2tKV, w2tKV + 131072, w2tC);
-
-    k_uvproj_s_nfa<<<3584, 256, 0, stream>>>(X, WuS, WvS, As, Upr, Vpr, nfS);
-    k_gemm_ntsk<<<dim3(8, 8, 4), 256, 0, stream>>>(Upr, Vpr, part, 512, 512, 1536, 384);
-    k_softmax_anpn<<<kN, 256, 0, stream>>>(part, As, nfS, Ps, AnS, PnS);
+    k_front<<<18392, 256, 0, stream>>>(
+        enc_gW, enc_cW, dec_gW, dec_cW, mfS_w2, mfC_w2,
+        X, WuS, WvS, As, WuC, WvC, featr,
+        WTg_e, WTc_e, WTg_d, WTc_d, w2tKV, w2tKV + 131072, w2tC,
+        Upr, Vpr, nfS, Uc, Vc, XHb, XHd, Ht);
+
+    k_p2<<<272, 256, 0, stream>>>(Upr, Vpr, part, Uc, Vc, Ac,
+                                  mfC_w1, mfC_b1, w2tC, mfC_b2, kvC);
+    k_p3<<<513, 256, 0, stream>>>(part, As, nfS, Ps, AnS, PnS, kvC, Uc, Vc, Ac, GcF);
     k_mlp1kv<<<2048, 256, 0, stream>>>(AnS, PnS, mfS_w1, mfS_b1, hidKV);
     k_ntsk_kv2<<<dim3(4, 8, 2), 256, 0, stream>>>(hidKV, w2tKV, mfS_b2, keyval);
     k_gemm_ntsk<<<dim3(8, 8, 2), 256, 0, stream>>>(keyval, keyval + 131072, part, 512, 512, 256, 128);
     k_fuse_transp<<<dim3(16, 16), dim3(32, 8), 0, stream>>>(part, As, Ps, GstB);
     k_cheby64<<<dim3(8, 8), 256, 0, stream>>>(GstB, GstB + 262144);
-
-    k_uvproj_c2<<<kBT, 512, 0, stream>>>(X, WuC, WvC, Uc, Vc);
-    k_catmlp4<<<dim3(2, 8), 256, 0, stream>>>(Uc, Vc, Ac, mfC_w1, mfC_b1, w2tC, mfC_b2, kvC);
-    k_gcfuse4<<<1, 256, 0, stream>>>(kvC, Uc, Vc, Ac, GcF);
-
-    k_build_init<<<12288, 256, 0, stream>>>(X, featr, XHb, XHd, Ht);
 
     for (int t = 0; t < kT; ++t) {
         if (t == 0)
@@ -820,9 +916,11 @@
                                                    nullptr, nullptr, nullptr, nullptr, nullptr, 0);
     }
 
-    k_t1m<CLP_DEC, PL_DEC, 16, 128><<<dim3(1, 4, 8), 256, 0, stream>>>(GstB, XHd, Yb);
     for (int hz = 0; hz < kHOR; ++hz) {
-        k_t1m<CLP_DEC, PL_DEC, 64, 0><<<dim3(4, 4, 8), 256, 0, stream>>>(GstB, XHd, Yb);
+        if (hz == 0)
+            k_t1m_decg<<<dim3(5, 4, 8), 256, 0, stream>>>(GstB, XHd, Yb);
+        else
+            k_t1m_decg<<<dim3(4, 4, 8), 256, 0, stream>>>(GstB, XHd, Yb);
         k_gg<PL_DEC, 9, 1, 4><<<dim3(2, 128), 256, 0, stream>>>(XHd, Yb, WTg_d, Gg);
         k_gates_ep<PL_DEC, 64><<<2048, 256, 0, stream>>>(Gg, GcF, dec_gb, Ht, updb, XHd);
         k_t1m<CLP_DEC, PL_DEC, 64, 64><<<dim3(4, 4, 8), 256, 0, stream>>>(GstB, XHd, Yb);
```
